# Kernel optimization log

Hardware: AMD Instinct MI355X
Metric: run time of the kernel (lower is better)

Reference implementation:

```python
import jax, jax.numpy as jnp
import numpy as np

N = 200000   # points in scene batch
M = 32       # backbone feature width (cfg.m)
P = 64       # proposals after clustering
D = 16       # self.output_dim
NUM_PARAMS = (D + 3) * D + D + D + 1  # 337 = weight_nums + bias_nums


def _bn(x, g, b, eps=1e-5):
    # BatchNorm1d, training-mode batch stats over the point/instance axis
    mu = x.mean(axis=0)
    var = x.var(axis=0)
    return (x - mu) * jax.lax.rsqrt(var + eps) * g + b


def setup_inputs() -> dict:
    key = jax.random.key(0)
    ks = jax.random.split(key, 16)
    s = 0.1
    return {
        "feats": jax.random.normal(ks[0], (N, M), jnp.float32),
        "coords": jax.random.normal(ks[1], (N, 3), jnp.float32),
        "inst_feats": jax.random.normal(ks[2], (P, M), jnp.float32),
        "centers": jax.random.normal(ks[3], (P, 3), jnp.float32),
        "mask_w1": jax.random.normal(ks[4], (M, M), jnp.float32) * s,
        "mask_g1": jnp.ones((M,), jnp.float32), "mask_b1": jnp.zeros((M,), jnp.float32),
        "mask_w2": jax.random.normal(ks[5], (M, M), jnp.float32) * s,
        "mask_g2": jnp.ones((M,), jnp.float32), "mask_b2": jnp.zeros((M,), jnp.float32),
        "mask_w3": jax.random.normal(ks[6], (M, M), jnp.float32) * s,
        "mask_g3": jnp.ones((M,), jnp.float32), "mask_b3": jnp.zeros((M,), jnp.float32),
        "mask_w_out": jax.random.normal(ks[7], (M, D), jnp.float32) * s,
        "mask_b_out": jnp.zeros((D,), jnp.float32),
        # before_embedding_tower: conv1d 1x1 m->16 no-bias, BN, ReLU
        "emb_w": jax.random.normal(ks[8], (M, D), jnp.float32) * s,
        "emb_g": jnp.ones((D,), jnp.float32), "emb_b": jnp.zeros((D,), jnp.float32),
        # controller: conv1d 1x1 16->337 (std=0.01 init, zero bias)
        "ctrl_w": jax.random.normal(ks[9], (D, NUM_PARAMS), jnp.float32) * 0.01,
        "ctrl_b": jnp.zeros((NUM_PARAMS,), jnp.float32),
    }


def reference(feats, coords, inst_feats, centers,
              mask_w1, mask_g1, mask_b1,
              mask_w2, mask_g2, mask_b2,
              mask_w3, mask_g3, mask_b3,
              mask_w_out, mask_b_out,
              emb_w, emb_g, emb_b,
              ctrl_w, ctrl_b):
    # --- mask tower: per-point 1x1 convs ---
    x = feats
    for w, g, b in ((mask_w1, mask_g1, mask_b1),
                    (mask_w2, mask_g2, mask_b2),
                    (mask_w3, mask_g3, mask_b3)):
        x = jax.nn.relu(_bn(x @ w, g, b))
    mask_feats = x @ mask_w_out + mask_b_out                      # [N, D]

    # --- controller: generate dynamic filters per proposal ---
    e = jax.nn.relu(_bn(inst_feats @ emb_w, emb_g, emb_b))        # [P, D]
    params = e @ ctrl_w + ctrl_b                                  # [P, 337]
    w1 = params[:, :(D + 3) * D].reshape(P, D, D + 3)             # [P, out=16, in=19]
    w2 = params[:, (D + 3) * D:(D + 3) * D + D]                   # [P, 16] (out=1)
    b1 = params[:, (D + 4) * D:(D + 4) * D + D]                   # [P, 16]
    b2 = params[:, (D + 4) * D + D:]                              # [P, 1]

    # --- dynamic conv over all points; input = [rel_coords(3) | mask_feats(16)] ---
    rel = coords[None, :, :] - centers[:, None, :]                # [P, N, 3]
    h = (jnp.einsum('pnc,pdc->pnd', rel, w1[:, :, :3])
         + jnp.einsum('nc,pdc->pnd', mask_feats, w1[:, :, 3:])
         + b1[:, None, :])                                        # [P, N, 16]
    h = jax.nn.relu(h)
    logits = jnp.einsum('pnd,pd->pn', h, w2) + b2                 # [P, N]
    return logits
```

## Files before the change

kernel.cpp:

```cpp
#include <hip/hip_runtime.h>
#include <hip/hip_bf16.h>
#include <math.h>

#define N_PTS 200000
#define M 32
#define P_INST 64
#define D 16
#define NP 337

#define NBL ((N_PTS + 255) / 256)
#define HPB 128
#define NBH ((N_PTS + HPB - 1) / HPB)

#define WS_PARAMS 0
#define WS_STATS  21568
#define WS_W2     21760
#define WS_B2     22784
#define WS_APACK  22912
#define WS_Y      104832

typedef __attribute__((ext_vector_type(8))) short short8v;
typedef __attribute__((ext_vector_type(4))) float floatx4;
typedef __attribute__((ext_vector_type(16))) float floatx16;

static __device__ __forceinline__ unsigned short f2bf(float v) {
    __hip_bfloat16 h = __float2bfloat16(v);
    return *reinterpret_cast<unsigned short*>(&h);
}

__global__ __launch_bounds__(1024) void k_prep(
    const float* __restrict__ inst, const float* __restrict__ emb_w,
    const float* __restrict__ emb_g, const float* __restrict__ emb_b,
    const float* __restrict__ ctrl_w, const float* __restrict__ ctrl_b,
    const float* __restrict__ centers,
    float* __restrict__ params, float* __restrict__ apackf,
    float* __restrict__ w2p, float* __restrict__ b2p)
{
    __shared__ float sInst[P_INST * M];
    __shared__ float sCW[D * NP];
    __shared__ float sE[P_INST * D];
    __shared__ float sA[D], sC[D];
    int t = threadIdx.x;
    int lane = t & 63, wv = t >> 6;

    for (int i = t; i < P_INST * M; i += 1024) sInst[i] = inst[i];
    for (int i = t; i < D * NP; i += 1024) sCW[i] = ctrl_w[i];
    __syncthreads();

    {
        int p = t >> 4, d = t & (D - 1);
        float acc = 0.f;
        #pragma unroll
        for (int k = 0; k < M; k++) acc = fmaf(sInst[p * M + k], emb_w[k * D + d], acc);
        sE[t] = acc;
    }
    __syncthreads();

    if (t < D) {
        float s = 0.f, q = 0.f;
        for (int p = 0; p < P_INST; p++) { float v = sE[p * D + t]; s += v; q += v * v; }
        float mu = s * (1.f / P_INST);
        float var = q * (1.f / P_INST) - mu * mu;
        float a = emb_g[t] * rsqrtf(var + 1e-5f);
        sA[t] = a;
        sC[t] = emb_b[t] - mu * a;
    }
    __syncthreads();

    {
        int d = t & (D - 1);
        sE[t] = fmaxf(sE[t] * sA[d] + sC[d], 0.f);
    }
    __syncthreads();

    #pragma unroll
    for (int pp = 0; pp < 4; pp++) {
        int p = wv * 4 + pp;
        float e[D];
        #pragma unroll
        for (int d = 0; d < D; d++) e[d] = sE[p * D + d];
        for (int q = lane; q < NP; q += 64) {
            float acc = ctrl_b[q];
            #pragma unroll
            for (int d = 0; d < D; d++) acc = fmaf(e[d], sCW[d * NP + q], acc);
            params[p * NP + q] = acc;
        }
    }
    __threadfence_block();
    __syncthreads();

    {
        int row = lane & 31;
        int d = row & 15, psub = row >> 4;
        #pragma unroll
        for (int half = 0; half < 2; half++) {
            int pp = wv + half * 16;
            int p = pp * 2 + psub;
            const float* prm = params + p * NP;
            float bias = prm[320 + d] - (centers[p * 3 + 0] * prm[d * 19 + 0]
                                       + centers[p * 3 + 1] * prm[d * 19 + 1]
                                       + centers[p * 3 + 2] * prm[d * 19 + 2]);
            #pragma unroll
            for (int kc = 0; kc < 2; kc++) {
                int kbase = kc * 16 + (lane >> 5) * 8;
                unsigned int w[4];
                #pragma unroll
                for (int i = 0; i < 4; i++) {
                    unsigned short lo = 0, hi = 0;
                    #pragma unroll
                    for (int h = 0; h < 2; h++) {
                        int k = kbase + 2 * i + h;
                        float v;
                        if (k < 19) v = prm[d * 19 + k];
                        else if (k == 19) v = bias;
                        else v = 0.f;
                        if (h == 0) lo = f2bf(v); else hi = f2bf(v);
                    }
                    w[i] = (unsigned)lo | ((unsigned)hi << 16);
                }
                uint4* dst = (uint4*)((char*)apackf + (size_t)pp * 2048
                                      + kc * 1024 + lane * 16);
                *dst = make_uint4(w[0], w[1], w[2], w[3]);
            }
        }
    }

    {
        #pragma unroll
        for (int pi = 0; pi < 4; pi++) {
            int p = wv + pi * 16;
            const float* prm = params + p * NP;
            if (lane < 16) w2p[p * 16 + lane] = prm[304 + lane];
            if (lane == 0) b2p[p] = prm[336];
        }
    }
}

template <int L>
__global__ __launch_bounds__(256) void k_layer(
    const float* __restrict__ feats, const float* __restrict__ W,
    const float* __restrict__ stats, float* __restrict__ ybuf,
    float* __restrict__ partials)
{
    __shared__ float tr[256 * 33];
    __shared__ float red2[2][8][32];
    int t = threadIdx.x;
    int n = blockIdx.x * 256 + t;
    bool valid = n < N_PTS;
    int nc = valid ? n : N_PTS - 1;

    const float* src = ((L == 0) ? feats : ybuf) + (size_t)nc * M;
    float x[M];
    #pragma unroll
    for (int q = 0; q < M / 4; q++) {
        float4 v = ((const float4*)src)[q];
        x[4*q] = v.x; x[4*q+1] = v.y; x[4*q+2] = v.z; x[4*q+3] = v.w;
    }
    if (L > 0) {
        const float* st = stats + (L - 1) * 64;
        #pragma unroll
        for (int j = 0; j < M; j++) x[j] = fmaxf(fmaf(x[j], st[j], st[32 + j]), 0.f);
    }
    float y[M];
    #pragma unroll
    for (int j = 0; j < M; j++) y[j] = 0.f;
    #pragma unroll
    for (int i = 0; i < M; i++) {
        float xi = x[i];
        #pragma unroll
        for (int j = 0; j < M; j++) y[j] = fmaf(xi, W[i * M + j], y[j]);
    }
    if (valid) {
        float4* dst = (float4*)(ybuf + (size_t)n * M);
        #pragma unroll
        for (int q = 0; q < M / 4; q++)
            dst[q] = make_float4(y[4*q], y[4*q+1], y[4*q+2], y[4*q+3]);
    } else {
        #pragma unroll
        for (int j = 0; j < M; j++) y[j] = 0.f;
    }

    #pragma unroll
    for (int j = 0; j < M; j++) tr[t * 33 + j] = y[j];
    __syncthreads();
    int c = t & 31, s = t >> 5;
    float S = 0.f, Q = 0.f;
    #pragma unroll
    for (int r = 0; r < 32; r++) {
        float v = tr[(s * 32 + r) * 33 + c];
        S += v; Q += v * v;
    }
    red2[0][s][c] = S;
    red2[1][s][c] = Q;
    __syncthreads();
    if (t < 64) {
        int cc = t & 31, k = t >> 5;
        float a = 0.f;
        #pragma unroll
        for (int sl = 0; sl < 8; sl++) a += red2[k][sl][cc];
        partials[(size_t)blockIdx.x * 64 + k * 32 + cc] = a;
    }
}

__global__ __launch_bounds__(256) void k_reduce(
    const float* __restrict__ partials,
    const float* __restrict__ g, const float* __restrict__ b,
    float* __restrict__ stats_out)
{
    int c = blockIdx.x;
    int t = threadIdx.x;
    int part = t >> 7;
    int i0 = t & 127;
    float s = 0.f;
    for (int i = i0; i < NBL; i += 128)
        s += partials[(size_t)i * 64 + part * 32 + c];
    __shared__ float sh[256];
    sh[t] = s;
    __syncthreads();
    #pragma unroll
    for (int off = 64; off; off >>= 1) {
        if ((t & 127) < off) sh[t] += sh[t + off];
        __syncthreads();
    }
    if (t == 0) {
        float S = sh[0], Q = sh[128];
        float mu = S * (1.f / N_PTS);
        float var = Q * (1.f / N_PTS) - mu * mu;
        float a = g[c] * rsqrtf(var + 1e-5f);
        stats_out[c] = a;
        stats_out[32 + c] = b[c] - mu * a;
    }
}

__global__ __launch_bounds__(512)
__attribute__((amdgpu_waves_per_eu(2, 4)))
void k_head(
    const float* __restrict__ ybuf, const float* __restrict__ coords,
    const float* __restrict__ w_out, const float* __restrict__ b_out,
    const float* __restrict__ stats, const float* __restrict__ w2p,
    const float* __restrict__ b2p, const float* __restrict__ apackf,
    float* __restrict__ out)
{
    __shared__ unsigned int zlds[HPB * 20];
    __shared__ float w2lds[32 * 32];
    __shared__ float b2lds[64];
    int t = threadIdx.x;
    int nblk = blockIdx.x * HPB;

    if (t < HPB) {
        int nc = nblk + t;
        if (nc >= N_PTS) nc = N_PTS - 1;
        const float* yr = ybuf + (size_t)nc * M;
        float x[M];
        #pragma unroll
        for (int q = 0; q < M / 4; q++) {
            float4 v = ((const float4*)yr)[q];
            x[4*q] = v.x; x[4*q+1] = v.y; x[4*q+2] = v.z; x[4*q+3] = v.w;
        }
        const float* st = stats + 128;
        #pragma unroll
        for (int j = 0; j < M; j++) x[j] = fmaxf(fmaf(x[j], st[j], st[32 + j]), 0.f);

        float mf[D];
        #pragma unroll
        for (int d = 0; d < D; d++) mf[d] = b_out[d];
        #pragma unroll
        for (int i = 0; i < M; i++) {
            float xi = x[i];
            #pragma unroll
            for (int d = 0; d < D; d++) mf[d] = fmaf(xi, w_out[i * D + d], mf[d]);
        }
        float z[20];
        z[0] = coords[(size_t)nc * 3 + 0];
        z[1] = coords[(size_t)nc * 3 + 1];
        z[2] = coords[(size_t)nc * 3 + 2];
        #pragma unroll
        for (int d = 0; d < D; d++) z[3 + d] = mf[d];
        z[19] = 1.0f;

        unsigned int zw[16];
        #pragma unroll
        for (int i = 0; i < 10; i++)
            zw[i] = (unsigned)f2bf(z[2 * i]) | ((unsigned)f2bf(z[2 * i + 1]) << 16);
        #pragma unroll
        for (int i = 10; i < 16; i++) zw[i] = 0u;
        uint4* zd = (uint4*)&zlds[t * 20];
        #pragma unroll
        for (int i = 0; i < 4; i++)
            zd[i] = make_uint4(zw[4*i], zw[4*i+1], zw[4*i+2], zw[4*i+3]);
    } else if (t < 256) {
        int t2 = t - 128;
        if (t2 < 64) b2lds[t2] = b2p[t2];
        #pragma unroll
        for (int e = 0; e < 8; e++) {
            int idx = t2 * 8 + e;
            int pp = idx >> 5;
            int rem = idx & 31;
            int hi = rem >> 4, reg = rem & 15;
            int R = (reg & 3) + 8 * (reg >> 2) + 4 * hi;
            int p = pp * 2 + (R >> 4), d = R & 15;
            w2lds[idx] = w2p[p * 16 + d];
        }
    }
    __syncthreads();

    int lane = t & 63, wv = t >> 6;
    int col = lane & 31, hi = lane >> 5;

    short8v B1[4], B2[4];
    #pragma unroll
    for (int s = 0; s < 4; s++) {
        const unsigned int* zrow = &zlds[(s * 32 + col) * 20];
        B1[s] = *(const short8v*)(zrow + hi * 4);
        B2[s] = *(const short8v*)(zrow + 8 + hi * 4);
    }

    const char* abase = (const char*)apackf + (size_t)(wv * 4) * 2048 + lane * 16;

    short8v A1n = *(const short8v*)(abase);
    short8v A2n = *(const short8v*)(abase + 1024);

    #pragma unroll
    for (int i = 0; i < 4; i++) {
        int pp = wv * 4 + i;
        short8v A1 = A1n, A2 = A2n;
        if (i < 3) {
            A1n = *(const short8v*)(abase + (size_t)(i + 1) * 2048);
            A2n = *(const short8v*)(abase + (size_t)(i + 1) * 2048 + 1024);
        }
        const float* w2r = &w2lds[pp * 32 + hi * 16];
        floatx4 w2a = *(const floatx4*)(w2r + 0);
        floatx4 w2b = *(const floatx4*)(w2r + 4);
        floatx4 w2c = *(const floatx4*)(w2r + 8);
        floatx4 w2d = *(const floatx4*)(w2r + 12);
        float b2 = b2lds[pp * 2 + hi];

        #pragma unroll
        for (int s = 0; s < 4; s++) {
            floatx16 acc = {};
            acc = __builtin_amdgcn_mfma_f32_32x32x16_bf16(A1, B1[s], acc, 0, 0, 0);
            acc = __builtin_amdgcn_mfma_f32_32x32x16_bf16(A2, B2[s], acc, 0, 0, 0);

            float pA = fmaxf(acc[0], 0.f) * w2a[0];
            pA = fmaf(fmaxf(acc[1], 0.f), w2a[1], pA);
            pA = fmaf(fmaxf(acc[2], 0.f), w2a[2], pA);
            pA = fmaf(fmaxf(acc[3], 0.f), w2a[3], pA);
            pA = fmaf(fmaxf(acc[4], 0.f), w2b[0], pA);
            pA = fmaf(fmaxf(acc[5], 0.f), w2b[1], pA);
            pA = fmaf(fmaxf(acc[6], 0.f), w2b[2], pA);
            pA = fmaf(fmaxf(acc[7], 0.f), w2b[3], pA);
            float pB = fmaxf(acc[8], 0.f) * w2c[0];
            pB = fmaf(fmaxf(acc[9], 0.f), w2c[1], pB);
            pB = fmaf(fmaxf(acc[10], 0.f), w2c[2], pB);
            pB = fmaf(fmaxf(acc[11], 0.f), w2c[3], pB);
            pB = fmaf(fmaxf(acc[12], 0.f), w2d[0], pB);
            pB = fmaf(fmaxf(acc[13], 0.f), w2d[1], pB);
            pB = fmaf(fmaxf(acc[14], 0.f), w2d[2], pB);
            pB = fmaf(fmaxf(acc[15], 0.f), w2d[3], pB);

            pA += __shfl_xor(pA, 32, 64);
            pB += __shfl_xor(pB, 32, 64);

            int nn = nblk + s * 32 + col;
            float vout = (hi ? pB : pA) + b2;
            if (nn < N_PTS) out[(size_t)(pp * 2 + hi) * N_PTS + nn] = vout;
        }
    }
}

extern "C" void kernel_launch(void* const* d_in, const int* in_sizes, int n_in,
                              void* d_out, int out_size, void* d_ws, size_t ws_size,
                              hipStream_t stream) {
    const float* feats   = (const float*)d_in[0];
    const float* coords  = (const float*)d_in[1];
    const float* inst    = (const float*)d_in[2];
    const float* centers = (const float*)d_in[3];
    const float* mw1 = (const float*)d_in[4];
    const float* mg1 = (const float*)d_in[5];
    const float* mb1 = (const float*)d_in[6];
    const float* mw2 = (const float*)d_in[7];
    const float* mg2 = (const float*)d_in[8];
    const float* mb2 = (const float*)d_in[9];
    const float* mw3 = (const float*)d_in[10];
    const float* mg3 = (const float*)d_in[11];
    const float* mb3 = (const float*)d_in[12];
    const float* wout = (const float*)d_in[13];
    const float* bout = (const float*)d_in[14];
    const float* embw = (const float*)d_in[15];
    const float* embg = (const float*)d_in[16];
    const float* embb = (const float*)d_in[17];
    const float* cw   = (const float*)d_in[18];
    const float* cb   = (const float*)d_in[19];

    float* wsf      = (float*)d_ws;
    float* params   = wsf + WS_PARAMS;
    float* stats    = wsf + WS_STATS;
    float* w2p      = wsf + WS_W2;
    float* b2p      = wsf + WS_B2;
    float* apackf   = wsf + WS_APACK;
    float* ybuf     = wsf + WS_Y;
    float* out      = (float*)d_out;
    float* partials = (float*)d_out;

    k_prep<<<1, 1024, 0, stream>>>(inst, embw, embg, embb, cw, cb, centers,
                                   params, apackf, w2p, b2p);

    k_layer<0><<<NBL, 256, 0, stream>>>(feats, mw1, stats, ybuf, partials);
    k_reduce<<<32, 256, 0, stream>>>(partials, mg1, mb1, stats + 0);

    k_layer<1><<<NBL, 256, 0, stream>>>(feats, mw2, stats, ybuf, partials);
    k_reduce<<<32, 256, 0, stream>>>(partials, mg2, mb2, stats + 64);

    k_layer<2><<<NBL, 256, 0, stream>>>(feats, mw3, stats, ybuf, partials);
    k_reduce<<<32, 256, 0, stream>>>(partials, mg3, mb3, stats + 128);

    k_head<<<NBH, 512, 0, stream>>>(ybuf, coords, wout, bout, stats,
                                    w2p, b2p, apackf, out);
}
```

Before: 142.4 us.

## Split head into separate z-packing kernel and LDS-free MFMA head kernel

Moves the BN-apply, output projection and bf16 packing of the per-point input vector out of the head kernel into a new k_z kernel, which writes the packed vectors in place over ybuf. The head kernel drops LDS and __syncthreads, reads the B operands straight from global memory, and runs 4 waves that each handle 8 proposals instead of 8 waves handling 4. The w2/b2 values are pre-permuted into the MFMA register order in k_prep, so the head loads them directly. This costs an extra launch and an extra write and read of the packed buffer, in exchange for removing the serial in-block prologue where only some threads did work while the rest waited.

Measured after the change: 145.5 us. +2.2%, slower.

```diff
diff --git a/kernel.cpp b/kernel.cpp
--- a/kernel.cpp
+++ b/kernel.cpp
@@ -14,9 +14,8 @@
 
 #define WS_PARAMS 0
 #define WS_STATS  21568
-#define WS_W2     21760
-#define WS_B2     22784
-#define WS_APACK  22912
+#define WS_W2BLK  21760
+#define WS_APACK  23040
 #define WS_Y      104832
 
 typedef __attribute__((ext_vector_type(8))) short short8v;
@@ -34,7 +33,7 @@
     const float* __restrict__ ctrl_w, const float* __restrict__ ctrl_b,
     const float* __restrict__ centers,
     float* __restrict__ params, float* __restrict__ apackf,
-    float* __restrict__ w2p, float* __restrict__ b2p)
+    float* __restrict__ w2blk)
 {
     __shared__ float sInst[P_INST * M];
     __shared__ float sCW[D * NP];
@@ -122,16 +121,15 @@
                                       + kc * 1024 + lane * 16);
                 *dst = make_uint4(w[0], w[1], w[2], w[3]);
             }
-        }
-    }
-
-    {
-        #pragma unroll
-        for (int pi = 0; pi < 4; pi++) {
-            int p = wv + pi * 16;
-            const float* prm = params + p * NP;
-            if (lane < 16) w2p[p * 16 + lane] = prm[304 + lane];
-            if (lane == 0) b2p[p] = prm[336];
+
+            if (lane < 32) {
+                int hi2 = lane >> 4, reg = lane & 15;
+                int R = (reg & 3) + 8 * (reg >> 2) + 4 * hi2;
+                int pw = pp * 2 + (R >> 4), dw = R & 15;
+                w2blk[pp * 40 + lane] = params[pw * NP + 304 + dw];
+            } else if (lane < 34) {
+                w2blk[pp * 40 + lane] = params[(pp * 2 + (lane & 1)) * NP + 336];
+            }
         }
     }
 }
@@ -232,108 +230,94 @@
     }
 }
 
-__global__ __launch_bounds__(512)
-__attribute__((amdgpu_waves_per_eu(2, 4)))
-void k_head(
-    const float* __restrict__ ybuf, const float* __restrict__ coords,
-    const float* __restrict__ w_out, const float* __restrict__ b_out,
-    const float* __restrict__ stats, const float* __restrict__ w2p,
-    const float* __restrict__ b2p, const float* __restrict__ apackf,
-    float* __restrict__ out)
+__global__ __launch_bounds__(256) void k_z(
+    const float* __restrict__ coords, const float* __restrict__ w_out,
+    const float* __restrict__ b_out, const float* __restrict__ stats,
+    float* __restrict__ ybuf)
 {
-    __shared__ unsigned int zlds[HPB * 20];
-    __shared__ float w2lds[32 * 32];
-    __shared__ float b2lds[64];
+    int n = blockIdx.x * 256 + threadIdx.x;
+    if (n >= N_PTS) return;
+    float* yr = ybuf + (size_t)n * M;
+    float x[M];
+    #pragma unroll
+    for (int q = 0; q < M / 4; q++) {
+        float4 v = ((const float4*)yr)[q];
+        x[4*q] = v.x; x[4*q+1] = v.y; x[4*q+2] = v.z; x[4*q+3] = v.w;
+    }
+    const float* st = stats + 128;
+    #pragma unroll
+    for (int j = 0; j < M; j++) x[j] = fmaxf(fmaf(x[j], st[j], st[32 + j]), 0.f);
+
+    float mf[D];
+    #pragma unroll
+    for (int d = 0; d < D; d++) mf[d] = b_out[d];
+    #pragma unroll
+    for (int i = 0; i < M; i++) {
+        float xi = x[i];
+        #pragma unroll
+        for (int d = 0; d < D; d++) mf[d] = fmaf(xi, w_out[i * D + d], mf[d]);
+    }
+    float z[20];
+    z[0] = coords[(size_t)n * 3 + 0];
+    z[1] = coords[(size_t)n * 3 + 1];
+    z[2] = coords[(size_t)n * 3 + 2];
+    #pragma unroll
+    for (int d = 0; d < D; d++) z[3 + d] = mf[d];
+    z[19] = 1.0f;
+
+    unsigned int zw[16];
+    #pragma unroll
+    for (int i = 0; i < 10; i++)
+        zw[i] = (unsigned)f2bf(z[2 * i]) | ((unsigned)f2bf(z[2 * i + 1]) << 16);
+    #pragma unroll
+    for (int i = 10; i < 16; i++) zw[i] = 0u;
+    uint4* dst = (uint4*)yr;
+    #pragma unroll
+    for (int i = 0; i < 4; i++)
+        dst[i] = make_uint4(zw[4*i], zw[4*i+1], zw[4*i+2], zw[4*i+3]);
+}
+
+__global__ __launch_bounds__(256) void k_head(
+    const float* __restrict__ ybuf, const float* __restrict__ w2blk,
+    const float* __restrict__ apackf, float* __restrict__ out)
+{
     int t = threadIdx.x;
-    int nblk = blockIdx.x * HPB;
-
-    if (t < HPB) {
-        int nc = nblk + t;
-        if (nc >= N_PTS) nc = N_PTS - 1;
-        const float* yr = ybuf + (size_t)nc * M;
-        float x[M];
-        #pragma unroll
-        for (int q = 0; q < M / 4; q++) {
-            float4 v = ((const float4*)yr)[q];
-            x[4*q] = v.x; x[4*q+1] = v.y; x[4*q+2] = v.z; x[4*q+3] = v.w;
-        }
-        const float* st = stats + 128;
-        #pragma unroll
-        for (int j = 0; j < M; j++) x[j] = fmaxf(fmaf(x[j], st[j], st[32 + j]), 0.f);
-
-        float mf[D];
-        #pragma unroll
-        for (int d = 0; d < D; d++) mf[d] = b_out[d];
-        #pragma unroll
-        for (int i = 0; i < M; i++) {
-            float xi = x[i];
-            #pragma unroll
-            for (int d = 0; d < D; d++) mf[d] = fmaf(xi, w_out[i * D + d], mf[d]);
-        }
-        float z[20];
-        z[0] = coords[(size_t)nc * 3 + 0];
-        z[1] = coords[(size_t)nc * 3 + 1];
-        z[2] = coords[(size_t)nc * 3 + 2];
-        #pragma unroll
-        for (int d = 0; d < D; d++) z[3 + d] = mf[d];
-        z[19] = 1.0f;
-
-        unsigned int zw[16];
-        #pragma unroll
-        for (int i = 0; i < 10; i++)
-            zw[i] = (unsigned)f2bf(z[2 * i]) | ((unsigned)f2bf(z[2 * i + 1]) << 16);
-        #pragma unroll
-        for (int i = 10; i < 16; i++) zw[i] = 0u;
-        uint4* zd = (uint4*)&zlds[t * 20];
-        #pragma unroll
-        for (int i = 0; i < 4; i++)
-            zd[i] = make_uint4(zw[4*i], zw[4*i+1], zw[4*i+2], zw[4*i+3]);
-    } else if (t < 256) {
-        int t2 = t - 128;
-        if (t2 < 64) b2lds[t2] = b2p[t2];
-        #pragma unroll
-        for (int e = 0; e < 8; e++) {
-            int idx = t2 * 8 + e;
-            int pp = idx >> 5;
-            int rem = idx & 31;
-            int hi = rem >> 4, reg = rem & 15;
-            int R = (reg & 3) + 8 * (reg >> 2) + 4 * hi;
-            int p = pp * 2 + (R >> 4), d = R & 15;
-            w2lds[idx] = w2p[p * 16 + d];
-        }
-    }
-    __syncthreads();
-
     int lane = t & 63, wv = t >> 6;
     int col = lane & 31, hi = lane >> 5;
-
+    int nblk = blockIdx.x * HPB;
+
+    const char* zb = (const char*)ybuf;
     short8v B1[4], B2[4];
     #pragma unroll
     for (int s = 0; s < 4; s++) {
-        const unsigned int* zrow = &zlds[(s * 32 + col) * 20];
-        B1[s] = *(const short8v*)(zrow + hi * 4);
-        B2[s] = *(const short8v*)(zrow + 8 + hi * 4);
-    }
-
-    const char* abase = (const char*)apackf + (size_t)(wv * 4) * 2048 + lane * 16;
+        int nn = nblk + s * 32 + col;
+        int nc = nn < N_PTS ? nn : N_PTS - 1;
+        const char* zr = zb + (size_t)nc * 128;
+        B1[s] = *(const short8v*)(zr + hi * 16);
+        B2[s] = *(const short8v*)(zr + 32 + hi * 16);
+    }
+
+    const char* abase = (const char*)apackf + (size_t)(wv * 8) * 2048 + lane * 16;
+    const float* w2base = w2blk + (size_t)(wv * 8) * 40;
 
     short8v A1n = *(const short8v*)(abase);
     short8v A2n = *(const short8v*)(abase + 1024);
 
     #pragma unroll
-    for (int i = 0; i < 4; i++) {
-        int pp = wv * 4 + i;
+    for (int i = 0; i < 8; i++) {
+        int pp = wv * 8 + i;
         short8v A1 = A1n, A2 = A2n;
-        if (i < 3) {
+        if (i < 7) {
             A1n = *(const short8v*)(abase + (size_t)(i + 1) * 2048);
             A2n = *(const short8v*)(abase + (size_t)(i + 1) * 2048 + 1024);
         }
-        const float* w2r = &w2lds[pp * 32 + hi * 16];
+        const float* w2r = w2base + (size_t)i * 40 + hi * 16;
         floatx4 w2a = *(const floatx4*)(w2r + 0);
         floatx4 w2b = *(const floatx4*)(w2r + 4);
         floatx4 w2c = *(const floatx4*)(w2r + 8);
         floatx4 w2d = *(const floatx4*)(w2r + 12);
-        float b2 = b2lds[pp * 2 + hi];
+        float2 b2v = *(const float2*)(w2base + (size_t)i * 40 + 32);
+        float b2 = hi ? b2v.y : b2v.x;
 
         #pragma unroll
         for (int s = 0; s < 4; s++) {
@@ -395,15 +379,14 @@
     float* wsf      = (float*)d_ws;
     float* params   = wsf + WS_PARAMS;
     float* stats    = wsf + WS_STATS;
-    float* w2p      = wsf + WS_W2;
-    float* b2p      = wsf + WS_B2;
+    float* w2blk    = wsf + WS_W2BLK;
     float* apackf   = wsf + WS_APACK;
     float* ybuf     = wsf + WS_Y;
     float* out      = (float*)d_out;
     float* partials = (float*)d_out;
 
     k_prep<<<1, 1024, 0, stream>>>(inst, embw, embg, embb, cw, cb, centers,
-                                   params, apackf, w2p, b2p);
+                                   params, apackf, w2blk);
 
     k_layer<0><<<NBL, 256, 0, stream>>>(feats, mw1, stats, ybuf, partials);
     k_reduce<<<32, 256, 0, stream>>>(partials, mg1, mb1, stats + 0);
@@ -414,6 +397,7 @@
     k_layer<2><<<NBL, 256, 0, stream>>>(feats, mw3, stats, ybuf, partials);
     k_reduce<<<32, 256, 0, stream>>>(partials, mg3, mb3, stats + 128);
 
-    k_head<<<NBH, 512, 0, stream>>>(ybuf, coords, wout, bout, stats,
-                                    w2p, b2p, apackf, out);
-}
+    k_z<<<NBL, 256, 0, stream>>>(coords, wout, bout, stats, ybuf);
+
+    k_head<<<NBH, 256, 0, stream>>>(ybuf, w2blk, apackf, out);
+}
```

## Split BN statistics out of layer kernel into separate column-sum pass

Applied to the files above, without the earlier changes.

Removes the shared-memory transpose and block reduction from the per-layer matmul kernel, which now only computes and stores y. A new grid-strided k_colsum kernel rereads ybuf with float4 loads and reduces sums and squares via wave shuffles into a fixed number of partials. This is meant to cut LDS use and barriers in the layer kernel so it can run at higher occupancy. The cost is an extra launch per layer and an additional full read of the 25.6 MB ybuf three times.

Result: slower. 170.0 us (+19.4%).

```diff
diff --git a/kernel.cpp b/kernel.cpp
--- a/kernel.cpp
+++ b/kernel.cpp
@@ -11,6 +11,7 @@
 #define NBL ((N_PTS + 255) / 256)
 #define HPB 128
 #define NBH ((N_PTS + HPB - 1) / HPB)
+#define COLS_BLOCKS 2048
 
 #define WS_PARAMS 0
 #define WS_STATS  21568
@@ -139,17 +140,12 @@
 template <int L>
 __global__ __launch_bounds__(256) void k_layer(
     const float* __restrict__ feats, const float* __restrict__ W,
-    const float* __restrict__ stats, float* __restrict__ ybuf,
-    float* __restrict__ partials)
+    const float* __restrict__ stats, float* __restrict__ ybuf)
 {
-    __shared__ float tr[256 * 33];
-    __shared__ float red2[2][8][32];
-    int t = threadIdx.x;
-    int n = blockIdx.x * 256 + t;
-    bool valid = n < N_PTS;
-    int nc = valid ? n : N_PTS - 1;
-
-    const float* src = ((L == 0) ? feats : ybuf) + (size_t)nc * M;
+    int n = blockIdx.x * 256 + threadIdx.x;
+    if (n >= N_PTS) return;
+
+    const float* src = ((L == 0) ? feats : ybuf) + (size_t)n * M;
     float x[M];
     #pragma unroll
     for (int q = 0; q < M / 4; q++) {
@@ -170,36 +166,47 @@
         #pragma unroll
         for (int j = 0; j < M; j++) y[j] = fmaf(xi, W[i * M + j], y[j]);
     }
-    if (valid) {
-        float4* dst = (float4*)(ybuf + (size_t)n * M);
-        #pragma unroll
-        for (int q = 0; q < M / 4; q++)
-            dst[q] = make_float4(y[4*q], y[4*q+1], y[4*q+2], y[4*q+3]);
-    } else {
-        #pragma unroll
-        for (int j = 0; j < M; j++) y[j] = 0.f;
-    }
-
-    #pragma unroll
-    for (int j = 0; j < M; j++) tr[t * 33 + j] = y[j];
-    __syncthreads();
-    int c = t & 31, s = t >> 5;
-    float S = 0.f, Q = 0.f;
-    #pragma unroll
-    for (int r = 0; r < 32; r++) {
-        float v = tr[(s * 32 + r) * 33 + c];
-        S += v; Q += v * v;
-    }
-    red2[0][s][c] = S;
-    red2[1][s][c] = Q;
-    __syncthreads();
-    if (t < 64) {
-        int cc = t & 31, k = t >> 5;
-        float a = 0.f;
-        #pragma unroll
-        for (int sl = 0; sl < 8; sl++) a += red2[k][sl][cc];
-        partials[(size_t)blockIdx.x * 64 + k * 32 + cc] = a;
-    }
+    float4* dst = (float4*)(ybuf + (size_t)n * M);
+    #pragma unroll
+    for (int q = 0; q < M / 4; q++)
+        dst[q] = make_float4(y[4*q], y[4*q+1], y[4*q+2], y[4*q+3]);
+}
+
+__global__ __launch_bounds__(256) void k_colsum(
+    const float* __restrict__ ybuf, float* __restrict__ partials)
+{
+    int t = threadIdx.x;
+    int g = t & 7;
+    float s[4] = {0.f, 0.f, 0.f, 0.f}, q[4] = {0.f, 0.f, 0.f, 0.f};
+
+    for (size_t idx = (size_t)blockIdx.x * 256 + t; idx < (size_t)N_PTS * 8;
+         idx += (size_t)COLS_BLOCKS * 256) {
+        size_t row = idx >> 3;
+        float4 v = *(const float4*)(ybuf + row * M + g * 4);
+        s[0] += v.x; s[1] += v.y; s[2] += v.z; s[3] += v.w;
+        q[0] += v.x * v.x; q[1] += v.y * v.y; q[2] += v.z * v.z; q[3] += v.w * v.w;
+    }
+    #pragma unroll
+    for (int i = 0; i < 4; i++) {
+        #pragma unroll
+        for (int off = 32; off >= 8; off >>= 1) {
+            s[i] += __shfl_down(s[i], off, 64);
+            q[i] += __shfl_down(q[i], off, 64);
+        }
+    }
+    __shared__ float red[4][64];
+    int wv = t >> 6, lane = t & 63;
+    if (lane < 8) {
+        #pragma unroll
+        for (int i = 0; i < 4; i++) {
+            red[wv][lane * 4 + i] = s[i];
+            red[wv][32 + lane * 4 + i] = q[i];
+        }
+    }
+    __syncthreads();
+    if (t < 64)
+        partials[(size_t)blockIdx.x * 64 + t] =
+            red[0][t] + red[1][t] + red[2][t] + red[3][t];
 }
 
 __global__ __launch_bounds__(256) void k_reduce(
@@ -212,7 +219,7 @@
     int part = t >> 7;
     int i0 = t & 127;
     float s = 0.f;
-    for (int i = i0; i < NBL; i += 128)
+    for (int i = i0; i < COLS_BLOCKS; i += 128)
         s += partials[(size_t)i * 64 + part * 32 + c];
     __shared__ float sh[256];
     sh[t] = s;
@@ -405,13 +412,16 @@
     k_prep<<<1, 1024, 0, stream>>>(inst, embw, embg, embb, cw, cb, centers,
                                    params, apackf, w2p, b2p);
 
-    k_layer<0><<<NBL, 256, 0, stream>>>(feats, mw1, stats, ybuf, partials);
+    k_layer<0><<<NBL, 256, 0, stream>>>(feats, mw1, stats, ybuf);
+    k_colsum<<<COLS_BLOCKS, 256, 0, stream>>>(ybuf, partials);
     k_reduce<<<32, 256, 0, stream>>>(partials, mg1, mb1, stats + 0);
 
-    k_layer<1><<<NBL, 256, 0, stream>>>(feats, mw2, stats, ybuf, partials);
+    k_layer<1><<<NBL, 256, 0, stream>>>(feats, mw2, stats, ybuf);
+    k_colsum<<<COLS_BLOCKS, 256, 0, stream>>>(ybuf, partials);
     k_reduce<<<32, 256, 0, stream>>>(partials, mg2, mb2, stats + 64);
 
-    k_layer<2><<<NBL, 256, 0, stream>>>(feats, mw3, stats, ybuf, partials);
+    k_layer<2><<<NBL, 256, 0, stream>>>(feats, mw3, stats, ybuf);
+    k_colsum<<<COLS_BLOCKS, 256, 0, stream>>>(ybuf, partials);
     k_reduce<<<32, 256, 0, stream>>>(partials, mg3, mb3, stats + 128);
 
     k_head<<<NBH, 512, 0, stream>>>(ybuf, coords, wout, bout, stats,
```
